# Kernel optimization log

Hardware: AMD Instinct MI355X
Metric: run time of the kernel (lower is better)

Reference implementation:

```python
import jax, jax.numpy as jnp
import numpy as np

N_EMBD = 2048
EPS = 1e-5

def layernorm(x, g, b):
    mu = jnp.mean(x, axis=-1, keepdims=True)
    var = jnp.mean(jnp.square(x - mu), axis=-1, keepdims=True)
    return (x - mu) * jax.lax.rsqrt(var + EPS) * g + b

def gelu_erf(x):
    return x * 0.5 * (1.0 + jax.lax.erf(x / jnp.sqrt(jnp.asarray(2.0, x.dtype))))

def setup_inputs() -> dict:
    key = jax.random.key(0)
    ks = jax.random.split(key, 2)
    x = jax.random.normal(ks[0], (4, 4096, N_EMBD), dtype=jnp.float32)
    W = jax.random.normal(ks[1], (N_EMBD, N_EMBD), dtype=jnp.float32) / np.sqrt(N_EMBD)
    bW = jnp.zeros((N_EMBD,), jnp.float32)
    g1 = jnp.ones((N_EMBD,), jnp.float32)
    b1 = jnp.zeros((N_EMBD,), jnp.float32)
    g2 = jnp.ones((N_EMBD,), jnp.float32)
    b2 = jnp.zeros((N_EMBD,), jnp.float32)
    return {"x": x, "W": W, "bW": bW, "g1": g1, "b1": b1, "g2": g2, "b2": b2}

def reference(x, W, bW, g1, b1, g2, b2):
    h = layernorm(x, g1, b1)                         # [B,S,D]
    h = jnp.einsum('bsd,ed->bse', h, W) + bW         # Linear(D,D)
    h = gelu_erf(h)
    return layernorm(h, g2, b2)
```

## Files before the change

### kernel.cpp

```cpp
#include <hip/hip_runtime.h>
#include <hip/hip_bf16.h>
#include <math.h>


#define D 2048
#define MROWS 16384
#define BMT 256
#define BNT 256
#define KTILES (D / 64)

typedef __bf16 bf16x8 __attribute__((ext_vector_type(8)));
typedef float f32x4 __attribute__((ext_vector_type(4)));

#define GLP(p) ((const __attribute__((address_space(1))) void*)(p))
#define LDSP(p) ((__attribute__((address_space(3))) void*)(p))
#define S_VMCNT(n) asm volatile("s_waitcnt vmcnt(" #n ")" ::: "memory")
#define MEMFENCE() asm volatile("" ::: "memory")
#define BAR() __builtin_amdgcn_s_barrier()
#define SCHED_FENCE() __builtin_amdgcn_sched_barrier(0)

__device__ __forceinline__ float gelu_f(float v) {
  return 0.5f * v * (1.0f + erff(v * 0.70710678118654752f));
}

__global__ __launch_bounds__(256) void ln1_kernel(
    const float* __restrict__ x, const float* __restrict__ g,
    const float* __restrict__ b, __hip_bfloat16* __restrict__ out) {
  const int tid = threadIdx.x;
  const size_t row = blockIdx.x;
  const float4* xr = (const float4*)(x + row * D);
  float4 v0 = xr[2 * tid];
  float4 v1 = xr[2 * tid + 1];
  float s  = v0.x + v0.y + v0.z + v0.w + v1.x + v1.y + v1.z + v1.w;
  float ss = v0.x*v0.x + v0.y*v0.y + v0.z*v0.z + v0.w*v0.w
           + v1.x*v1.x + v1.y*v1.y + v1.z*v1.z + v1.w*v1.w;
#pragma unroll
  for (int off = 32; off > 0; off >>= 1) {
    s  += __shfl_down(s, off, 64);
    ss += __shfl_down(ss, off, 64);
  }
  __shared__ float red[8];
  const int w = tid >> 6;
  if ((tid & 63) == 0) { red[w] = s; red[w + 4] = ss; }
  __syncthreads();
  s  = red[0] + red[1] + red[2] + red[3];
  ss = red[4] + red[5] + red[6] + red[7];
  const float mu  = s * (1.0f / D);
  const float var = ss * (1.0f / D) - mu * mu;
  const float inv = rsqrtf(var + 1e-5f);
  const float4* gv = (const float4*)g;
  const float4* bv = (const float4*)b;
  float4 g0 = gv[2 * tid], g1 = gv[2 * tid + 1];
  float4 b0 = bv[2 * tid], b1 = bv[2 * tid + 1];
  alignas(16) __hip_bfloat16 h[8];
  h[0] = __float2bfloat16((v0.x - mu) * inv * g0.x + b0.x);
  h[1] = __float2bfloat16((v0.y - mu) * inv * g0.y + b0.y);
  h[2] = __float2bfloat16((v0.z - mu) * inv * g0.z + b0.z);
  h[3] = __float2bfloat16((v0.w - mu) * inv * g0.w + b0.w);
  h[4] = __float2bfloat16((v1.x - mu) * inv * g1.x + b1.x);
  h[5] = __float2bfloat16((v1.y - mu) * inv * g1.y + b1.y);
  h[6] = __float2bfloat16((v1.z - mu) * inv * g1.z + b1.z);
  h[7] = __float2bfloat16((v1.w - mu) * inv * g1.w + b1.w);
  *(uint4*)(out + row * D + (size_t)tid * 8) = *(const uint4*)h;
}

__global__ __launch_bounds__(256) void cvt_kernel(
    const float* __restrict__ W, __hip_bfloat16* __restrict__ Wb, int n8) {
  const int i = blockIdx.x * 256 + threadIdx.x;
  if (i >= n8) return;
  const float4* p = (const float4*)W + 2 * (size_t)i;
  float4 a = p[0], c = p[1];
  alignas(16) __hip_bfloat16 h[8] = {
      __float2bfloat16(a.x), __float2bfloat16(a.y),
      __float2bfloat16(a.z), __float2bfloat16(a.w),
      __float2bfloat16(c.x), __float2bfloat16(c.y),
      __float2bfloat16(c.z), __float2bfloat16(c.w)};
  *(uint4*)(Wb + (size_t)i * 8) = *(const uint4*)h;
}

__global__ __launch_bounds__(512, 2) void gemm_kernel(
    const __hip_bfloat16* __restrict__ A,
    const __hip_bfloat16* __restrict__ Bw,
    const float* __restrict__ bias,
    float* __restrict__ C) {
  __shared__ __hip_bfloat16 sA[2 * 2 * 256 * 32];
  __shared__ __hip_bfloat16 sB[2 * 2 * 256 * 32];
  const int tid = threadIdx.x;
  const int l = tid & 63;
  const int wid = tid >> 6;
  const int fr = l & 15;
  const int lk = l >> 4;
  const size_t m0 = (size_t)blockIdx.x * BMT;
  const int n0 = blockIdx.y * BNT;
  const int whm = wid >> 2;
  const int wn = (wid & 3) * 64;
  char* const ldsA = (char*)sA;
  char* const ldsB = (char*)sB;

  const int slot = ((2 * lk + (fr & 1)) ^ (fr >> 1)) << 4;
  const int aoff = whm * 8192 + (fr >> 1) * 128 + slot;
  const int boff = wn * 64 + (fr >> 1) * 128 + slot;

  const int line = tid >> 3;
  const int v = (tid & 7) ^ (line & 7);
  const int srow0 = 2 * line + (v & 1);
  const int srow1 = srow0 + 128;
  const int scol = (v >> 1) * 8;
  const int ldd0 = tid * 16;
  const int ldd1 = ldd0 + 8192;
  const __hip_bfloat16* const Ag = A + m0 * D;
  const __hip_bfloat16* const Bg = Bw + (size_t)n0 * D;

  auto stg = [&](char* lds, const __hip_bfloat16* G, int so, int kh, int kt) {
    const __hip_bfloat16* s0 = G + (size_t)srow0 * D + kt * 64 + kh * 32 + scol;
    const __hip_bfloat16* s1 = G + (size_t)srow1 * D + kt * 64 + kh * 32 + scol;
    char* q = lds + (so << 15) + (kh << 14);
    __builtin_amdgcn_global_load_lds(GLP(s0), LDSP(q + ldd0), 16, 0, 0);
    __builtin_amdgcn_global_load_lds(GLP(s1), LDSP(q + ldd1), 16, 0, 0);
  };

  bf16x8 a[8], b[4];
  f32x4 acc[8][4] = {};

  auto rd = [&](int bo, int kh) {
    const char* pa = ldsA + bo + (kh << 14) + aoff;
    const char* pb = ldsB + bo + (kh << 14) + boff;
#pragma unroll
    for (int mi = 0; mi < 8; ++mi) a[mi] = *(const bf16x8*)(pa + mi * 1024);
#pragma unroll
    for (int ni = 0; ni < 4; ++ni) b[ni] = *(const bf16x8*)(pb + ni * 1024);
  };
  auto mma = [&]() {
    __builtin_amdgcn_s_setprio(1);
#pragma unroll
    for (int mi = 0; mi < 8; ++mi)
#pragma unroll
      for (int ni = 0; ni < 4; ++ni)
        acc[mi][ni] = __builtin_amdgcn_mfma_f32_16x16x32_bf16(a[mi], b[ni], acc[mi][ni], 0, 0, 0);
    __builtin_amdgcn_s_setprio(0);
  };

  stg(ldsA, Ag, 0, 0, 0); stg(ldsB, Bg, 0, 0, 0);
  stg(ldsA, Ag, 0, 1, 0); stg(ldsB, Bg, 0, 1, 0);

  for (int kt = 0; kt < KTILES - 1; ++kt) {
    const int bo = (kt & 1) << 15;
    const int so = (kt & 1) ^ 1;
    S_VMCNT(4);
    BAR(); MEMFENCE(); SCHED_FENCE();
    rd(bo, 0);
    stg(ldsA, Ag, so, 0, kt + 1); stg(ldsB, Bg, so, 0, kt + 1);
    mma();
    S_VMCNT(4);
    BAR(); MEMFENCE(); SCHED_FENCE();
    rd(bo, 1);
    stg(ldsA, Ag, so, 1, kt + 1); stg(ldsB, Bg, so, 1, kt + 1);
    mma();
  }
  {
    const int bo = ((KTILES - 1) & 1) << 15;
    S_VMCNT(4);
    BAR(); MEMFENCE(); SCHED_FENCE();
    rd(bo, 0);
    mma();
    S_VMCNT(0);
    BAR(); MEMFENCE(); SCHED_FENCE();
    rd(bo, 1);
    mma();
  }

  float bv[4];
#pragma unroll
  for (int ni = 0; ni < 4; ++ni) bv[ni] = bias[n0 + wn + ni * 16 + fr];
#pragma unroll
  for (int mi = 0; mi < 8; ++mi) {
    const size_t rbase = m0 + whm * 128 + mi * 16 + lk * 4;
#pragma unroll
    for (int rr = 0; rr < 4; ++rr) {
      float* crow = C + (rbase + rr) * D + n0 + wn + fr;
#pragma unroll
      for (int ni = 0; ni < 4; ++ni)
        crow[ni * 16] = gelu_f(acc[mi][ni][rr] + bv[ni]);
    }
  }
}

__global__ __launch_bounds__(256) void ln2_kernel(
    float* __restrict__ C, const float* __restrict__ g, const float* __restrict__ b) {
  const int tid = threadIdx.x;
  const size_t row = blockIdx.x;
  float4* cr = (float4*)(C + row * D);
  float4 v0 = cr[2 * tid], v1 = cr[2 * tid + 1];
  float s  = v0.x + v0.y + v0.z + v0.w + v1.x + v1.y + v1.z + v1.w;
  float ss = v0.x*v0.x + v0.y*v0.y + v0.z*v0.z + v0.w*v0.w
           + v1.x*v1.x + v1.y*v1.y + v1.z*v1.z + v1.w*v1.w;
#pragma unroll
  for (int off = 32; off > 0; off >>= 1) {
    s  += __shfl_down(s, off, 64);
    ss += __shfl_down(ss, off, 64);
  }
  __shared__ float red[8];
  const int w = tid >> 6;
  if ((tid & 63) == 0) { red[w] = s; red[w + 4] = ss; }
  __syncthreads();
  s  = red[0] + red[1] + red[2] + red[3];
  ss = red[4] + red[5] + red[6] + red[7];
  const float mu  = s * (1.0f / D);
  const float var = ss * (1.0f / D) - mu * mu;
  const float inv = rsqrtf(var + 1e-5f);
  const float4* gv = (const float4*)g;
  const float4* bv = (const float4*)b;
  float4 g0 = gv[2 * tid], g1 = gv[2 * tid + 1];
  float4 b0 = bv[2 * tid], b1 = bv[2 * tid + 1];
  float4 o0, o1;
  o0.x = (v0.x - mu) * inv * g0.x + b0.x;
  o0.y = (v0.y - mu) * inv * g0.y + b0.y;
  o0.z = (v0.z - mu) * inv * g0.z + b0.z;
  o0.w = (v0.w - mu) * inv * g0.w + b0.w;
  o1.x = (v1.x - mu) * inv * g1.x + b1.x;
  o1.y = (v1.y - mu) * inv * g1.y + b1.y;
  o1.z = (v1.z - mu) * inv * g1.z + b1.z;
  o1.w = (v1.w - mu) * inv * g1.w + b1.w;
  cr[2 * tid] = o0;
  cr[2 * tid + 1] = o1;
}

extern "C" void kernel_launch(void* const* d_in, const int* in_sizes, int n_in,
                              void* d_out, int out_size, void* d_ws, size_t ws_size,
                              hipStream_t stream) {
  const float* x  = (const float*)d_in[0];
  const float* W  = (const float*)d_in[1];
  const float* bW = (const float*)d_in[2];
  const float* g1 = (const float*)d_in[3];
  const float* b1 = (const float*)d_in[4];
  const float* g2 = (const float*)d_in[5];
  const float* b2 = (const float*)d_in[6];
  float* out = (float*)d_out;

  __hip_bfloat16* Abf = (__hip_bfloat16*)d_ws;
  __hip_bfloat16* Wbf = Abf + (size_t)MROWS * D;

  ln1_kernel<<<MROWS, 256, 0, stream>>>(x, g1, b1, Abf);
  cvt_kernel<<<(D * D / 8) / 256, 256, 0, stream>>>(W, Wbf, D * D / 8);
  dim3 grid(MROWS / BMT, D / BNT);
  gemm_kernel<<<grid, 512, 0, stream>>>(Abf, Wbf, bW, out);
  ln2_kernel<<<MROWS, 256, 0, stream>>>(out, g2, b2);
}
```

Baseline: 233.7 us.

## Replace double-buffered GEMM K loop with 4-stage ring of 32-wide slices

The GEMM main loop now streams K in 32-wide slices through a 4-slot LDS ring and keeps three slices in flight, waiting on vmcnt(8) instead of double-buffering 64-wide tiles split into halves. The LDS layout also changes from an XOR-swizzled arrangement to a fragment-native order, so each lane's ds_read is contiguous and the address math is simpler. The aim is to hide more global-load latency behind the MFMA work. LDS footprint and barrier count per slice stay the same, but the deeper prefetch keeps more loads outstanding.

```diff
diff --git a/kernel.cpp b/kernel.cpp
--- a/kernel.cpp
+++ b/kernel.cpp
@@ -7,7 +7,7 @@
 #define MROWS 16384
 #define BMT 256
 #define BNT 256
-#define KTILES (D / 64)
+#define NSLICES 64
 
 typedef __bf16 bf16x8 __attribute__((ext_vector_type(8)));
 typedef float f32x4 __attribute__((ext_vector_type(4)));
@@ -83,8 +83,8 @@
     const __hip_bfloat16* __restrict__ Bw,
     const float* __restrict__ bias,
     float* __restrict__ C) {
-  __shared__ __hip_bfloat16 sA[2 * 2 * 256 * 32];
-  __shared__ __hip_bfloat16 sB[2 * 2 * 256 * 32];
+  __shared__ __hip_bfloat16 sA[4 * 8192];
+  __shared__ __hip_bfloat16 sB[4 * 8192];
   const int tid = threadIdx.x;
   const int l = tid & 63;
   const int wid = tid >> 6;
@@ -94,37 +94,30 @@
   const int n0 = blockIdx.y * BNT;
   const int whm = wid >> 2;
   const int wn = (wid & 3) * 64;
-  char* const ldsA = (char*)sA;
-  char* const ldsB = (char*)sB;
-
-  const int slot = ((2 * lk + (fr & 1)) ^ (fr >> 1)) << 4;
-  const int aoff = whm * 8192 + (fr >> 1) * 128 + slot;
-  const int boff = wn * 64 + (fr >> 1) * 128 + slot;
-
-  const int line = tid >> 3;
-  const int v = (tid & 7) ^ (line & 7);
-  const int srow0 = 2 * line + (v & 1);
-  const int srow1 = srow0 + 128;
-  const int scol = (v >> 1) * 8;
-  const int ldd0 = tid * 16;
-  const int ldd1 = ldd0 + 8192;
-  const __hip_bfloat16* const Ag = A + m0 * D;
-  const __hip_bfloat16* const Bg = Bw + (size_t)n0 * D;
-
-  auto stg = [&](char* lds, const __hip_bfloat16* G, int so, int kh, int kt) {
-    const __hip_bfloat16* s0 = G + (size_t)srow0 * D + kt * 64 + kh * 32 + scol;
-    const __hip_bfloat16* s1 = G + (size_t)srow1 * D + kt * 64 + kh * 32 + scol;
-    char* q = lds + (so << 15) + (kh << 14);
-    __builtin_amdgcn_global_load_lds(GLP(s0), LDSP(q + ldd0), 16, 0, 0);
-    __builtin_amdgcn_global_load_lds(GLP(s1), LDSP(q + ldd1), 16, 0, 0);
+
+  const int srow = (tid >> 6) * 16 + (tid & 15);
+  const int scol = ((tid >> 4) & 3) * 8;
+  const int ldd = tid * 16;
+  const __hip_bfloat16* const Ag = A + m0 * D + (size_t)srow * D + scol;
+  const __hip_bfloat16* const Bg = Bw + (size_t)n0 * D + (size_t)srow * D + scol;
+
+  auto stg = [&](int s) {
+    const int kb = s * 32;
+    const int ro = (s & 3) << 14;
+    __builtin_amdgcn_global_load_lds(GLP(Ag + kb), LDSP((char*)sA + ro + ldd), 16, 0, 0);
+    __builtin_amdgcn_global_load_lds(GLP(Ag + (size_t)128 * D + kb), LDSP((char*)sA + ro + 8192 + ldd), 16, 0, 0);
+    __builtin_amdgcn_global_load_lds(GLP(Bg + kb), LDSP((char*)sB + ro + ldd), 16, 0, 0);
+    __builtin_amdgcn_global_load_lds(GLP(Bg + (size_t)128 * D + kb), LDSP((char*)sB + ro + 8192 + ldd), 16, 0, 0);
   };
 
   bf16x8 a[8], b[4];
   f32x4 acc[8][4] = {};
-
-  auto rd = [&](int bo, int kh) {
-    const char* pa = ldsA + bo + (kh << 14) + aoff;
-    const char* pb = ldsB + bo + (kh << 14) + boff;
+  const int abase = whm * 8192 + l * 16;
+  const int bbase = (wid & 3) * 4096 + l * 16;
+
+  auto rd = [&](int s) {
+    const char* pa = (const char*)sA + ((s & 3) << 14) + abase;
+    const char* pb = (const char*)sB + ((s & 3) << 14) + bbase;
 #pragma unroll
     for (int mi = 0; mi < 8; ++mi) a[mi] = *(const bf16x8*)(pa + mi * 1024);
 #pragma unroll
@@ -140,34 +133,18 @@
     __builtin_amdgcn_s_setprio(0);
   };
 
-  stg(ldsA, Ag, 0, 0, 0); stg(ldsB, Bg, 0, 0, 0);
-  stg(ldsA, Ag, 0, 1, 0); stg(ldsB, Bg, 0, 1, 0);
-
-  for (int kt = 0; kt < KTILES - 1; ++kt) {
-    const int bo = (kt & 1) << 15;
-    const int so = (kt & 1) ^ 1;
-    S_VMCNT(4);
+  stg(0); stg(1); stg(2);
+
+  for (int p = 0; p < 61; ++p) {
+    S_VMCNT(8);
     BAR(); MEMFENCE(); SCHED_FENCE();
-    rd(bo, 0);
-    stg(ldsA, Ag, so, 0, kt + 1); stg(ldsB, Bg, so, 0, kt + 1);
+    stg(p + 3);
+    rd(p);
     mma();
-    S_VMCNT(4);
-    BAR(); MEMFENCE(); SCHED_FENCE();
-    rd(bo, 1);
-    stg(ldsA, Ag, so, 1, kt + 1); stg(ldsB, Bg, so, 1, kt + 1);
-    mma();
-  }
-  {
-    const int bo = ((KTILES - 1) & 1) << 15;
-    S_VMCNT(4);
-    BAR(); MEMFENCE(); SCHED_FENCE();
-    rd(bo, 0);
-    mma();
-    S_VMCNT(0);
-    BAR(); MEMFENCE(); SCHED_FENCE();
-    rd(bo, 1);
-    mma();
-  }
+  }
+  S_VMCNT(8);  BAR(); MEMFENCE(); SCHED_FENCE(); rd(61); mma();
+  S_VMCNT(4);  BAR(); MEMFENCE(); SCHED_FENCE(); rd(62); mma();
+  S_VMCNT(0);  BAR(); MEMFENCE(); SCHED_FENCE(); rd(63); mma();
 
   float bv[4];
 #pragma unroll
```

After: 305.0 us. +30.5%, slower.
